# Kernel optimization log

Measured on AMD Instinct MI355X. Metric: run time of the kernel, lower is better.

## Reference

```python
import jax, jax.numpy as jnp
import numpy as np

SEQ, BATCH, HID, OUT = 2048, 128, 256, 2

def setup_inputs() -> dict:
    key = jax.random.key(0)
    ks = jax.random.split(key, 6)
    return {
        "x": jax.random.normal(ks[0], (SEQ, BATCH), dtype=jnp.float32),
        # torch code draws h inside forward: randn*0.01 + 0.5 -> pass as input for determinism
        "h0": jax.random.normal(ks[1], (BATCH, HID), dtype=jnp.float32) * 0.01 + 0.5,
        "W_ih": jax.random.normal(ks[2], (HID, 1), dtype=jnp.float32) * 0.05 + 0.4,
        "W_hh": jax.random.normal(ks[3], (HID, HID), dtype=jnp.float32) * 0.2,
        "W_hh_bias": jax.random.normal(ks[4], (HID, HID), dtype=jnp.float32) * 0.01 + 0.5,
        "b_h": jnp.zeros((HID,), dtype=jnp.float32),
        "W": jax.random.normal(ks[5], (OUT, HID), dtype=jnp.float32) * 0.1 + 0.5,
        "b": jnp.zeros((OUT,), dtype=jnp.float32),
        "context": 1,
    }

def reference(x, h0, W_ih, W_hh, W_hh_bias, b_h, W, b, context):
    # context is a scalar, so c1 + c2 = (2h-1) @ (W_hh + context*W_hh_bias).T (same math, one GEMM)
    W_eff = W_hh + context * W_hh_bias            # (hid, hid)
    w_in = W_ih[:, 0]                             # input_size == 1 -> (hid,)

    def step(h, x_t):
        # c0: (batch,1)@(1,hid) == outer product of x_t with W_ih column
        pre = x_t[:, None] * w_in[None, :] + (2.0 * h - 1.0) @ W_eff.T + b_h
        h_new = jax.nn.sigmoid(pre)
        return h_new, h_new

    _, hs = jax.lax.scan(step, h0, x)             # hs: (seq, batch, hid)
    out = jnp.transpose(hs, (1, 0, 2))            # (batch, seq, hid)
    y = out @ W.T + b                             # (batch, seq, out)
    return y[:, :, 0], out
```

## Files before the change

kernel.cpp:

```cpp
#include <hip/hip_runtime.h>
#include <math.h>

#define SEQ   2048
#define BATCH 128
#define HID   256
#define OUTD  2
#define NW    8
#define KS    (HID / NW)

__global__ __launch_bounds__(512, 2)
void rnn_scan_kernel(const float* __restrict__ x,
                     const float* __restrict__ h0,
                     const float* __restrict__ W_ih,
                     const float* __restrict__ W_hh,
                     const float* __restrict__ W_hh_b,
                     const float* __restrict__ b_h,
                     const int*   __restrict__ context,
                     float*       __restrict__ out_hs)
{
    const int b   = blockIdx.x;
    const int tid = threadIdx.x;
    const int w   = tid >> 6;
    const int l   = tid & 63;

    __shared__ __align__(16) float v_lds[HID];
    __shared__ __align__(16) float part[NW][HID];
    __shared__ float x_lds[SEQ];

    for (int t = tid; t < SEQ; t += 512)
        x_lds[t] = x[t * BATCH + b];

    const float ctx = (float)context[0];

    float4 wr_[4][8];
    #pragma unroll
    for (int i = 0; i < 4; ++i) {
        const float* wp = W_hh   + (size_t)(4 * l + i) * HID + KS * w;
        const float* bp = W_hh_b + (size_t)(4 * l + i) * HID + KS * w;
        #pragma unroll
        for (int c = 0; c < 8; ++c) {
            const float4 a = *(const float4*)(wp + 4 * c);
            const float4 d = *(const float4*)(bp + 4 * c);
            wr_[i][c] = make_float4(a.x + ctx * d.x, a.y + ctx * d.y,
                                    a.z + ctx * d.z, a.w + ctx * d.w);
        }
    }

    float h = 0.f, winj = 0.f, bhj = 0.f;
    if (tid < HID) {
        h    = h0[(size_t)b * HID + tid];
        winj = W_ih[tid];
        bhj  = b_h[tid];
        v_lds[tid] = 2.f * h - 1.f;
    }
    float* outp = out_hs + (size_t)b * SEQ * HID + tid;

    __syncthreads();

    const float4* vbuf = (const float4*)v_lds + w * (KS / 4);

    for (int t = 0; t < SEQ; ++t) {
        float p0 = 0.f, p1 = 0.f, p2 = 0.f, p3 = 0.f;
        #pragma unroll
        for (int c = 0; c < 8; ++c) {
            const float4 v4 = vbuf[c];
            const float4 w0 = wr_[0][c];
            const float4 w1 = wr_[1][c];
            const float4 w2 = wr_[2][c];
            const float4 w3 = wr_[3][c];
            p0 += w0.x * v4.x; p0 += w0.y * v4.y; p0 += w0.z * v4.z; p0 += w0.w * v4.w;
            p1 += w1.x * v4.x; p1 += w1.y * v4.y; p1 += w1.z * v4.z; p1 += w1.w * v4.w;
            p2 += w2.x * v4.x; p2 += w2.y * v4.y; p2 += w2.z * v4.z; p2 += w2.w * v4.w;
            p3 += w3.x * v4.x; p3 += w3.y * v4.y; p3 += w3.z * v4.z; p3 += w3.w * v4.w;
        }
        *(float4*)(&part[w][4 * l]) = make_float4(p0, p1, p2, p3);

        __syncthreads();

        if (tid < HID) {
            const float s = ((part[0][tid] + part[1][tid]) +
                             (part[2][tid] + part[3][tid])) +
                            ((part[4][tid] + part[5][tid]) +
                             (part[6][tid] + part[7][tid]));
            const float pre = s + bhj + x_lds[t] * winj;
            h = 1.f / (1.f + __expf(-pre));
            v_lds[tid] = 2.f * h - 1.f;
            outp[(size_t)t * HID] = h;
        }
        __syncthreads();
    }
}

__global__ __launch_bounds__(256, 4)
void head_kernel(const float* __restrict__ hs,
                 const float* __restrict__ W,
                 const float* __restrict__ bias,
                 float*       __restrict__ y)
{
    const int lane   = threadIdx.x & 63;
    const int gwave  = (blockIdx.x * blockDim.x + threadIdx.x) >> 6;
    const int nwaves = (gridDim.x * blockDim.x) >> 6;

    const float4 w0 = *(const float4*)(W + lane * 4);
    const float  b0 = bias[0];

    const int nrows = BATCH * SEQ;
    for (int r = gwave; r < nrows; r += nwaves) {
        const float4 hv = *(const float4*)(hs + (size_t)r * HID + lane * 4);
        float s = hv.x * w0.x + hv.y * w0.y + hv.z * w0.z + hv.w * w0.w;
        #pragma unroll
        for (int off = 32; off; off >>= 1)
            s += __shfl_xor(s, off, 64);
        if (lane == 0) y[r] = s + b0;
    }
}

extern "C" void kernel_launch(void* const* d_in, const int* in_sizes, int n_in,
                              void* d_out, int out_size, void* d_ws, size_t ws_size,
                              hipStream_t stream) {
    const float* x      = (const float*)d_in[0];
    const float* h0     = (const float*)d_in[1];
    const float* W_ih   = (const float*)d_in[2];
    const float* W_hh   = (const float*)d_in[3];
    const float* W_hh_b = (const float*)d_in[4];
    const float* b_h    = (const float*)d_in[5];
    const float* W      = (const float*)d_in[6];
    const float* bias   = (const float*)d_in[7];
    const int*   ctx    = (const int*)d_in[8];

    float* y  = (float*)d_out;
    float* hs = y + (size_t)BATCH * SEQ;

    rnn_scan_kernel<<<BATCH, 512, 0, stream>>>(x, h0, W_ih, W_hh, W_hh_b,
                                               b_h, ctx, hs);
    head_kernel<<<2048, 256, 0, stream>>>(hs, W, bias, y);
}
```

Measured before the change: 1.513 ms.

## Reduce RNN scan to one barrier per step via shuffle-based partial-sum reduction

The recurrent kernel now runs 256 threads per batch element. Each thread holds an 8-row by 32-column slice of the effective weight matrix in registers and reduces partial sums across the 8 k-chunk lanes with a transpose-style xor-shuffle tree. This removes the LDS partial-sum buffer and one of the two barriers per timestep, using a padded double-buffered state vector instead. The head kernel is also reworked so each wave processes four rows at a time with 16-lane reductions. The cost is 256 float registers of weights per thread and fewer waves per block, which raises register pressure and risks spills.

```diff
diff --git a/kernel.cpp b/kernel.cpp
--- a/kernel.cpp
+++ b/kernel.cpp
@@ -4,11 +4,9 @@
 #define SEQ   2048
 #define BATCH 128
 #define HID   256
-#define OUTD  2
-#define NW    8
-#define KS    (HID / NW)
+#define VPAD  36
 
-__global__ __launch_bounds__(512, 2)
+__global__ __launch_bounds__(256, 1)
 void rnn_scan_kernel(const float* __restrict__ x,
                      const float* __restrict__ h0,
                      const float* __restrict__ W_ih,
@@ -20,73 +18,74 @@
 {
     const int b   = blockIdx.x;
     const int tid = threadIdx.x;
-    const int w   = tid >> 6;
-    const int l   = tid & 63;
+    const int rg  = tid >> 3;
+    const int kc  = tid & 7;
 
-    __shared__ __align__(16) float v_lds[HID];
-    __shared__ __align__(16) float part[NW][HID];
+    __shared__ __align__(16) float v_lds[2][8 * VPAD];
     __shared__ float x_lds[SEQ];
 
-    for (int t = tid; t < SEQ; t += 512)
+    for (int t = tid; t < SEQ; t += 256)
         x_lds[t] = x[t * BATCH + b];
 
     const float ctx = (float)context[0];
 
-    float4 wr_[4][8];
+    float4 wreg[8][8];
     #pragma unroll
-    for (int i = 0; i < 4; ++i) {
-        const float* wp = W_hh   + (size_t)(4 * l + i) * HID + KS * w;
-        const float* bp = W_hh_b + (size_t)(4 * l + i) * HID + KS * w;
+    for (int j = 0; j < 8; ++j) {
+        const int row = 8 * rg + (kc ^ j);
+        const float* wp = W_hh   + (size_t)row * HID + 32 * kc;
+        const float* bp = W_hh_b + (size_t)row * HID + 32 * kc;
         #pragma unroll
         for (int c = 0; c < 8; ++c) {
             const float4 a = *(const float4*)(wp + 4 * c);
             const float4 d = *(const float4*)(bp + 4 * c);
-            wr_[i][c] = make_float4(a.x + ctx * d.x, a.y + ctx * d.y,
-                                    a.z + ctx * d.z, a.w + ctx * d.w);
+            wreg[j][c] = make_float4(a.x + ctx * d.x, a.y + ctx * d.y,
+                                     a.z + ctx * d.z, a.w + ctx * d.w);
         }
     }
 
-    float h = 0.f, winj = 0.f, bhj = 0.f;
-    if (tid < HID) {
-        h    = h0[(size_t)b * HID + tid];
-        winj = W_ih[tid];
-        bhj  = b_h[tid];
-        v_lds[tid] = 2.f * h - 1.f;
-    }
+    float h = h0[(size_t)b * HID + tid];
+    const float winj = W_ih[tid];
+    const float bhj  = b_h[tid];
+
+    const int vslot = VPAD * (tid >> 5) + (tid & 31);
+    v_lds[0][vslot] = 2.f * h - 1.f;
+
     float* outp = out_hs + (size_t)b * SEQ * HID + tid;
+    const float4* vb0 = (const float4*)(v_lds[0] + VPAD * kc);
+    const float4* vb1 = (const float4*)(v_lds[1] + VPAD * kc);
 
     __syncthreads();
 
-    const float4* vbuf = (const float4*)v_lds + w * (KS / 4);
+    for (int t = 0; t < SEQ; ++t) {
+        const float4* vb = (t & 1) ? vb1 : vb0;
 
-    for (int t = 0; t < SEQ; ++t) {
-        float p0 = 0.f, p1 = 0.f, p2 = 0.f, p3 = 0.f;
+        float q[8] = {0.f, 0.f, 0.f, 0.f, 0.f, 0.f, 0.f, 0.f};
         #pragma unroll
         for (int c = 0; c < 8; ++c) {
-            const float4 v4 = vbuf[c];
-            const float4 w0 = wr_[0][c];
-            const float4 w1 = wr_[1][c];
-            const float4 w2 = wr_[2][c];
-            const float4 w3 = wr_[3][c];
-            p0 += w0.x * v4.x; p0 += w0.y * v4.y; p0 += w0.z * v4.z; p0 += w0.w * v4.w;
-            p1 += w1.x * v4.x; p1 += w1.y * v4.y; p1 += w1.z * v4.z; p1 += w1.w * v4.w;
-            p2 += w2.x * v4.x; p2 += w2.y * v4.y; p2 += w2.z * v4.z; p2 += w2.w * v4.w;
-            p3 += w3.x * v4.x; p3 += w3.y * v4.y; p3 += w3.z * v4.z; p3 += w3.w * v4.w;
+            const float4 v4 = vb[c];
+            #pragma unroll
+            for (int j = 0; j < 8; ++j) {
+                const float4 w = wreg[j][c];
+                q[j] += w.x * v4.x;
+                q[j] += w.y * v4.y;
+                q[j] += w.z * v4.z;
+                q[j] += w.w * v4.w;
+            }
         }
-        *(float4*)(&part[w][4 * l]) = make_float4(p0, p1, p2, p3);
+        q[0] += __shfl_xor(q[4], 4, 64);
+        q[1] += __shfl_xor(q[5], 4, 64);
+        q[2] += __shfl_xor(q[6], 4, 64);
+        q[3] += __shfl_xor(q[7], 4, 64);
+        q[0] += __shfl_xor(q[2], 2, 64);
+        q[1] += __shfl_xor(q[3], 2, 64);
+        q[0] += __shfl_xor(q[1], 1, 64);
 
-        __syncthreads();
+        const float pre = q[0] + bhj + x_lds[t] * winj;
+        h = 1.f / (1.f + __expf(-pre));
+        outp[(size_t)t * HID] = h;
+        v_lds[(t + 1) & 1][vslot] = 2.f * h - 1.f;
 
-        if (tid < HID) {
-            const float s = ((part[0][tid] + part[1][tid]) +
-                             (part[2][tid] + part[3][tid])) +
-                            ((part[4][tid] + part[5][tid]) +
-                             (part[6][tid] + part[7][tid]));
-            const float pre = s + bhj + x_lds[t] * winj;
-            h = 1.f / (1.f + __expf(-pre));
-            v_lds[tid] = 2.f * h - 1.f;
-            outp[(size_t)t * HID] = h;
-        }
         __syncthreads();
     }
 }
@@ -97,21 +96,36 @@
                  const float* __restrict__ bias,
                  float*       __restrict__ y)
 {
-    const int lane   = threadIdx.x & 63;
-    const int gwave  = (blockIdx.x * blockDim.x + threadIdx.x) >> 6;
-    const int nwaves = (gridDim.x * blockDim.x) >> 6;
+    const int tid  = threadIdx.x;
+    const int lane = tid & 63;
+    const int sub  = lane & 15;
+    const int rsub = lane >> 4;
 
-    const float4 w0 = *(const float4*)(W + lane * 4);
-    const float  b0 = bias[0];
+    float4 w0[4];
+    #pragma unroll
+    for (int u = 0; u < 4; ++u)
+        w0[u] = *(const float4*)(W + 4 * (16 * u + sub));
+    const float b0 = bias[0];
 
-    const int nrows = BATCH * SEQ;
-    for (int r = gwave; r < nrows; r += nwaves) {
-        const float4 hv = *(const float4*)(hs + (size_t)r * HID + lane * 4);
-        float s = hv.x * w0.x + hv.y * w0.y + hv.z * w0.z + hv.w * w0.w;
+    const int gwave = (blockIdx.x * blockDim.x + tid) >> 6;
+    const int nw    = (gridDim.x * blockDim.x) >> 6;
+    const int nq    = (BATCH * SEQ) >> 2;
+
+    for (int q = gwave; q < nq; q += nw) {
+        const int row = q * 4 + rsub;
+        const float* rp = hs + (size_t)row * HID;
+        float s = 0.f;
         #pragma unroll
-        for (int off = 32; off; off >>= 1)
-            s += __shfl_xor(s, off, 64);
-        if (lane == 0) y[r] = s + b0;
+        for (int u = 0; u < 4; ++u) {
+            const float4 hv = *(const float4*)(rp + 4 * (16 * u + sub));
+            s += hv.x * w0[u].x + hv.y * w0[u].y +
+                 hv.z * w0[u].z + hv.w * w0[u].w;
+        }
+        s += __shfl_xor(s, 1, 64);
+        s += __shfl_xor(s, 2, 64);
+        s += __shfl_xor(s, 4, 64);
+        s += __shfl_xor(s, 8, 64);
+        if (sub == 0) y[row] = s + b0;
     }
 }
 
@@ -131,7 +145,7 @@
     float* y  = (float*)d_out;
     float* hs = y + (size_t)BATCH * SEQ;
 
-    rnn_scan_kernel<<<BATCH, 512, 0, stream>>>(x, h0, W_ih, W_hh, W_hh_b,
+    rnn_scan_kernel<<<BATCH, HID, 0, stream>>>(x, h0, W_ih, W_hh, W_hh_b,
                                                b_h, ctx, hs);
     head_kernel<<<2048, 256, 0, stream>>>(hs, W, bias, y);
 }
```

New measurement: 2.508 ms. +65.8%, slower.
